# Performance work log

Hardware: AMD Instinct MI355X
Metric: run time of the kernel (lower is better)

Reference implementation:

```python
import jax, jax.numpy as jnp
import numpy as np

B, T, NQ, H = 32, 64, 128, 128


def setup_inputs() -> dict:
    key = jax.random.key(0)
    ks = jax.random.split(key, 16)
    n = lambda k, s, sc=0.05: jax.random.normal(k, s, dtype=jnp.float32) * sc
    return {
        "q": jax.random.randint(ks[0], (B, T), 0, NQ),
        "r": jax.random.randint(ks[1], (B, T), 0, 2),
        "x_emb_table": n(ks[2], (2 * NQ, H)),
        "q_emb": n(ks[3], (NQ, H)),
        "init_h": n(ks[4], (NQ, H)),
        "w1": n(ks[5], (H, 2 * H)),
        "b1": n(ks[6], (H,)),
        "w2": n(ks[7], (H, H)),
        "b2": n(ks[8], (H,)),
        "w_ih": n(ks[9], (3 * H, 2 * H)),
        "w_hh": n(ks[10], (3 * H, H)),
        "b_ih": n(ks[11], (3 * H,)),
        "b_hh": n(ks[12], (3 * H,)),
        "bias": n(ks[13], (1, NQ, 1)),
        "out_w": n(ks[14], (1, H)),
    }


def _gru_over_nodes(u, w_ih, w_hh, b_ih, b_hh):
    # Faithful to torch nn.GRU(batch_first=True) applied to [B, NQ, 2H]:
    # it recurs over the num_q axis with h0 = 0.
    h_dim = w_hh.shape[1]
    gi = jnp.einsum('bni,gi->bng', u, w_ih) + b_ih  # [B, NQ, 3H], input part precomputed

    def step(h, gi_t):  # h: [B, H], gi_t: [B, 3H]
        gh = h @ w_hh.T + b_hh
        ir, iz, inn = jnp.split(gi_t, 3, axis=-1)
        hr, hz, hn = jnp.split(gh, 3, axis=-1)
        rg = jax.nn.sigmoid(ir + hr)
        zg = jax.nn.sigmoid(iz + hz)
        ng = jnp.tanh(inn + rg * hn)
        h_new = (1.0 - zg) * ng + zg * h
        return h_new, h_new

    h0 = jnp.zeros((u.shape[0], h_dim), u.dtype)
    _, hs = jax.lax.scan(step, h0, jnp.swapaxes(gi, 0, 1))  # over NQ
    return jnp.swapaxes(hs, 0, 1)  # [B, NQ, H]


def reference(q, r, x_emb_table, q_emb, init_h, w1, b1, w2, b2,
              w_ih, w_hh, b_ih, b_hh, bias, out_w):
    bsz = q.shape[0]
    nq, hdim = q_emb.shape
    x = q + nq * r                                  # [B, T]
    x_emb = x_emb_table[x]                          # [B, T, H]
    qoh = jax.nn.one_hot(q, nq, dtype=x_emb.dtype)  # [B, T, NQ]
    ht0 = jnp.broadcast_to(init_h[None], (bsz, nq, hdim))

    def step(ht, inputs):
        xt, mask = inputs                # xt: [B,H], mask: [B,NQ]
        m3 = mask[..., None]             # [B, NQ, 1]
        # aggregate: second half is xt where qt matches, else q_emb; first half is ht either way
        other = m3 * xt[:, None, :] + (1.0 - m3) * q_emb[None]
        ht_ = jnp.concatenate([ht, other], axis=-1)          # [B, NQ, 2H]
        # update: f_neighbor is unimplemented (None->0); m = onehot * f_self(ht_)
        hs_mlp = jax.nn.relu(ht_ @ w1.T + b1) @ w2.T + b2    # mlp (eval: dropout=id)
        m = m3 * hs_mlp
        u = jnp.concatenate([m, ht], axis=-1)                # [B, NQ, 2H]
        ht_new = _gru_over_nodes(u, w_ih, w_hh, b_ih, b_hh)  # [B, NQ, H]
        yt = jax.nn.sigmoid(jnp.squeeze(ht_new @ out_w.T + bias, -1))  # [B, NQ]
        return ht_new, (ht_new, yt)

    _, (hs, ys) = jax.lax.scan(
        step, ht0, (jnp.swapaxes(x_emb, 0, 1), jnp.swapaxes(qoh, 0, 1)))
    h = jnp.concatenate([ht0[:, None], jnp.swapaxes(hs, 0, 1)], axis=1)  # [B, T+1, NQ, H]
    y = jnp.swapaxes(ys, 0, 1)                                           # [B, T, NQ]
    return y, h
```

## Files before the change

kernel.cpp:

```cpp
#include <hip/hip_runtime.h>

#define BB 32
#define TT 64
#define NQl 128
#define HD 128
#define CPAD 524
#define HPAD 132

#define SLOT_BYTES 8192
#define WS_FLAGS 8192
#define WS_SLOTS_OFF 16384
#define WS_NEED (WS_SLOTS_OFF + (size_t)NQl * SLOT_BYTES)

typedef _Float16 f16x8 __attribute__((ext_vector_type(8)));
typedef float f32x16 __attribute__((ext_vector_type(16)));
typedef float f32x4 __attribute__((ext_vector_type(4)));
typedef unsigned int u32x4 __attribute__((ext_vector_type(4)));
typedef int i32x4 __attribute__((ext_vector_type(4)));

__device__ __forceinline__ float sigmoidf_(float x) {
  return __builtin_amdgcn_rcpf(1.f + __expf(-x));
}
__device__ __forceinline__ float tanhf_(float x) {
  float a = fminf(fabsf(x), 15.f);
  float e = __expf(-2.f * a);
  float t = (1.f - e) * __builtin_amdgcn_rcpf(1.f + e);
  return copysignf(t, x);
}
__device__ __forceinline__ float dot4_(f32x4 a, f32x4 b) {
  return a[0] * b[0] + a[1] * b[1] + a[2] * b[2] + a[3] * b[3];
}
__device__ __forceinline__ f16x8 pack_frag_h(f32x4 a, f32x4 b) {
  f16x8 o;
  o[0] = (_Float16)a[0]; o[1] = (_Float16)a[1];
  o[2] = (_Float16)a[2]; o[3] = (_Float16)a[3];
  o[4] = (_Float16)b[0]; o[5] = (_Float16)b[1];
  o[6] = (_Float16)b[2]; o[7] = (_Float16)b[3];
  return o;
}
__device__ __forceinline__ u32x4 pack8_h(const float v[8]) {
  union { f16x8 h; u32x4 u; } c;
#pragma unroll
  for (int i = 0; i < 8; ++i) c.h[i] = (_Float16)v[i];
  return c.u;
}

__device__ __forceinline__ void bar_lds() {
  asm volatile("s_waitcnt lgkmcnt(0)" ::: "memory");
  __builtin_amdgcn_s_barrier();
  __builtin_amdgcn_sched_barrier(0);
}

__device__ __forceinline__ void issue_load32_cc(const float* p, f32x4& a, f32x4& b) {
  asm volatile(
      "global_load_dwordx4 %0, %2, off sc1\n\t"
      "global_load_dwordx4 %1, %2, off offset:16 sc1"
      : "=&v"(a), "=&v"(b) : "v"(p) : "memory");
}
__device__ __forceinline__ void wait_vm0_2(f32x4& a, f32x4& b) {
  asm volatile("s_waitcnt vmcnt(0)" : "+v"(a), "+v"(b) :: "memory");
  __builtin_amdgcn_sched_barrier(0);
}
__device__ __forceinline__ void store32_cc(float* p, f32x4 a, f32x4 b) {
  asm volatile(
      "global_store_dwordx4 %0, %1, off sc1\n\t"
      "global_store_dwordx4 %0, %2, off offset:16 sc1"
      :: "v"(p), "v"(a), "v"(b) : "memory");
}
__device__ __forceinline__ void issue_load16_cc(const void* p, u32x4& a) {
  asm volatile("global_load_dwordx4 %0, %1, off sc1" : "=&v"(a) : "v"(p) : "memory");
}
__device__ __forceinline__ void wait_vm0_1(u32x4& a) {
  asm volatile("s_waitcnt vmcnt(0)" : "+v"(a) :: "memory");
  __builtin_amdgcn_sched_barrier(0);
}
__device__ __forceinline__ void store16_cc(void* p, u32x4 v) {
  asm volatile("global_store_dwordx4 %0, %1, off sc1" :: "v"(p), "v"(v) : "memory");
}
__device__ __forceinline__ void store_flag_cc(int* p, int v) {
  asm volatile("global_store_dword %0, %1, off sc1" :: "v"(p), "v"(v) : "memory");
}
__device__ __forceinline__ int flagline_min(const int* p) {
  i32x4 a, b;
  asm volatile(
      "global_load_dwordx4 %0, %2, off sc1\n\t"
      "global_load_dwordx4 %1, %2, off offset:16 sc1\n\t"
      "s_waitcnt vmcnt(0)"
      : "=&v"(a), "=&v"(b) : "v"(p) : "memory");
  int m0 = min(min(a[0], a[1]), min(a[2], a[3]));
  int m1 = min(min(b[0], b[1]), min(b[2], b[3]));
  return min(m0, m1);
}

__global__ void __launch_bounds__(512, 2) gkt_wavefront(
    const int* __restrict__ qp, const int* __restrict__ rp_,
    const float* __restrict__ x_emb, const float* __restrict__ init_h,
    const float* __restrict__ w1, const float* __restrict__ b1,
    const float* __restrict__ w2, const float* __restrict__ b2,
    const float* __restrict__ w_ih, const float* __restrict__ w_hh,
    const float* __restrict__ b_ih, const float* __restrict__ b_hh,
    const float* __restrict__ bias, const float* __restrict__ out_w,
    float* __restrict__ y_out, float* h_out, int* wsbase,
    unsigned char* slots, int fastws) {
  __shared__ __align__(16) unsigned char smA[32 * 512];
  __shared__ float sC[32 * CPAD];
  __shared__ float sHrun[32 * HPAD];
  __shared__ float sHtp[2][32 * HPAD];
  __shared__ float sXt[32 * 128];
  __shared__ float sRed[4 * HPAD];
  __shared__ float sV1[128], sV2[128];
  __shared__ float sBias[128], sOutW[128], sB1[128], sB2[128];
  __shared__ unsigned int sMask[128];
  __shared__ int sTicket;

  const int tid = threadIdx.x;
  const int lane = tid & 63;
  const int wv = tid >> 6;
  const int l31 = lane & 31;
  const int lhi = lane >> 5;

  int* ticket = wsbase + 2048;
  if (tid == 0) sTicket = atomicAdd(ticket, 1);
  __syncthreads();
  const int t = sTicket;

  int* myFlagWord = (int*)((char*)wsbase + (size_t)t * 128) + wv;
  const int* parentLine = (const int*)((char*)wsbase + (size_t)(t - 1) * 128);

  if (tid < 128) {
    sBias[tid] = bias[tid];
    sOutW[tid] = out_w[tid];
    sB1[tid] = b1[tid];
    sB2[tid] = b2[tid];
    sMask[tid] = 0u;
  }
  for (int i = tid; i < 32 * HPAD; i += 512) sHrun[i] = 0.f;
  __syncthreads();
  if (tid < 32) {
    int qb = qp[tid * TT + t];
    atomicOr(&sMask[qb], 1u << tid);
  }

  const int b = tid >> 4;
  const int f = tid & 15;
  const unsigned int swzb = (unsigned int)((b & 7) << 4);
  const unsigned int imgOff = (unsigned int)(b * 256) + (((unsigned int)(f * 16)) ^ swzb);
  {
    int qb = qp[b * TT + t];
    int rb = rp_[b * TT + t];
    const float* src = x_emb + (size_t)(qb + NQl * rb) * HD + f * 8;
    *(f32x4*)(sXt + b * 128 + f * 8) = *(const f32x4*)src;
    *(f32x4*)(sXt + b * 128 + f * 8 + 4) = *(const f32x4*)(src + 4);
    *(u32x4*)(smA + b * 512 + ((unsigned int)(256 + f * 16) ^ swzb)) = (u32x4)(0u);
  }

  const int gcol = wv * 32 + l31;
  f16x8 Brz[16];
#pragma unroll
  for (int ks = 0; ks < 16; ++ks) {
    const float* src = (ks < 8)
        ? (w_ih + (size_t)gcol * 256 + 128 + ks * 16 + lhi * 8)
        : (w_hh + (size_t)gcol * 128 + (ks - 8) * 16 + lhi * 8);
    Brz[ks] = pack_frag_h(*(const f32x4*)src, *(const f32x4*)(src + 4));
  }
  const int ecol = (wv < 4) ? (256 + wv * 32 + l31) : (384 + (wv - 4) * 32 + l31);
  const int erow = (wv < 4) ? ecol : (ecol - 128);
  f16x8 Bex[8];
#pragma unroll
  for (int ks = 0; ks < 8; ++ks) {
    const float* src = (wv < 4)
        ? (w_ih + (size_t)erow * 256 + 128 + ks * 16 + lhi * 8)
        : (w_hh + (size_t)erow * 128 + ks * 16 + lhi * 8);
    Bex[ks] = pack_frag_h(*(const f32x4*)src, *(const f32x4*)(src + 4));
  }
  const float brz = b_ih[gcol] + b_hh[gcol];
  const float bex = (wv < 4) ? b_ih[ecol] : b_hh[erow];

  float* hstore_base = h_out + (((size_t)b * (TT + 1) + (t + 1)) * NQl) * HD + f * 8;
  const float* hload_base = h_out + (((size_t)b * (TT + 1) + t) * NQl) * HD + f * 8;

  {
    const f32x4* s4 = (const f32x4*)init_h;
    for (int i = t * 512 + tid; i < 32 * 4096; i += TT * 512) {
      int bb = i >> 12, rem = i & 4095;
      ((f32x4*)(h_out + ((size_t)bb * (TT + 1)) * NQl * HD))[rem] = s4[rem];
    }
  }

  {
    if (t > 0) {
      if (lane == 0) {
        int c = 0;
        while (flagline_min(parentLine) < 1) {
          if (++c > (1 << 17)) break;
        }
      }
      if (fastws) {
        u32x4 pv;
        issue_load16_cc(slots + imgOff, pv);
        wait_vm0_1(pv);
        *(u32x4*)(smA + b * 512 + (((unsigned int)(f * 16)) ^ swzb)) = pv;
        union { u32x4 u; _Float16 h[8]; } cc; cc.u = pv;
#pragma unroll
        for (int i = 0; i < 8; ++i) sHtp[0][b * HPAD + f * 8 + i] = (float)cc.h[i];
      } else {
        f32x4 a0, a1;
        issue_load32_cc(hload_base, a0, a1);
        wait_vm0_2(a0, a1);
        float v[8];
        *(f32x4*)&v[0] = a0; *(f32x4*)&v[4] = a1;
        *(f32x4*)(sHtp[0] + b * HPAD + f * 8) = a0;
        *(f32x4*)(sHtp[0] + b * HPAD + f * 8 + 4) = a1;
        *(u32x4*)(smA + b * 512 + (((unsigned int)(f * 16)) ^ swzb)) = pack8_h(v);
      }
    } else {
      float v[8];
      const float* src = init_h + f * 8;
      *(f32x4*)&v[0] = *(const f32x4*)src;
      *(f32x4*)&v[4] = *(const f32x4*)(src + 4);
      *(f32x4*)(sHtp[0] + b * HPAD + f * 8) = *(f32x4*)&v[0];
      *(f32x4*)(sHtp[0] + b * HPAD + f * 8 + 4) = *(f32x4*)&v[4];
      *(u32x4*)(smA + b * 512 + (((unsigned int)(f * 16)) ^ swzb)) = pack8_h(v);
    }
  }

  const int rowbase = l31 * 512;
  const unsigned int swz = (unsigned int)((l31 & 7) << 4);

  for (int n = 0; n < NQl; ++n) {
    bar_lds();

    f16x8 av[16];
#pragma unroll
    for (int ks = 0; ks < 16; ++ks) {
      unsigned int off = ((unsigned int)(ks * 32 + (lhi << 4))) ^ swz;
      av[ks] = *(const f16x8*)(smA + rowbase + off);
    }
    f32x16 accR, accE;
#pragma unroll
    for (int i = 0; i < 16; ++i) { accR[i] = brz; accE[i] = bex; }
#pragma unroll
    for (int ks = 0; ks < 16; ++ks)
      accR = __builtin_amdgcn_mfma_f32_32x32x16_f16(av[ks], Brz[ks], accR, 0, 0, 0);
    if (wv < 4) {
#pragma unroll
      for (int ks = 0; ks < 8; ++ks)
        accE = __builtin_amdgcn_mfma_f32_32x32x16_f16(av[ks], Bex[ks], accE, 0, 0, 0);
    } else {
#pragma unroll
      for (int ks = 0; ks < 8; ++ks)
        accE = __builtin_amdgcn_mfma_f32_32x32x16_f16(av[8 + ks], Bex[ks], accE, 0, 0, 0);
    }
#pragma unroll
    for (int rg = 0; rg < 16; ++rg) {
      int br = (rg & 3) + 8 * (rg >> 2) + 4 * lhi;
      sC[br * CPAD + gcol] = accR[rg];
      sC[br * CPAD + ecol] = accE[rg];
    }
    bar_lds();

    unsigned int mk = sMask[n];
    while (mk) {
      const int b0 = __ffs(mk) - 1;
      mk &= mk - 1;
      const float* htp_row = sHtp[n & 1] + b0 * HPAD;
      {
        const int j = tid & 127, kq = tid >> 7;
        const float* wr = w1 + (size_t)j * 256 + kq * 64;
        const float* xr = (kq < 2) ? (htp_row + kq * 64)
                                   : (sXt + b0 * 128 + (kq - 2) * 64);
        float s = 0.f;
#pragma unroll
        for (int ii = 0; ii < 16; ++ii)
          s += dot4_(*(const f32x4*)(wr + ii * 4), *(const f32x4*)(xr + ii * 4));
        sRed[kq * HPAD + j] = s;
      }
      bar_lds();
      if (tid < 128) {
        float v = sB1[tid] + sRed[tid] + sRed[HPAD + tid] + sRed[2 * HPAD + tid] +
                  sRed[3 * HPAD + tid];
        sV1[tid] = fmaxf(v, 0.f);
      }
      bar_lds();
      {
        const int j = tid & 127, kq = tid >> 7;
        const float* wr = w2 + (size_t)j * 128 + kq * 32;
        const float* xr = sV1 + kq * 32;
        float s = 0.f;
#pragma unroll
        for (int ii = 0; ii < 8; ++ii)
          s += dot4_(*(const f32x4*)(wr + ii * 4), *(const f32x4*)(xr + ii * 4));
        sRed[kq * HPAD + j] = s;
      }
      bar_lds();
      if (tid < 128)
        sV2[tid] = sB2[tid] + sRed[tid] + sRed[HPAD + tid] + sRed[2 * HPAD + tid] +
                   sRed[3 * HPAD + tid];
      bar_lds();
      if (tid < 384) {
        const float* wr = w_ih + (size_t)tid * 256;
        float s = 0.f;
#pragma unroll
        for (int ii = 0; ii < 32; ++ii)
          s += dot4_(*(const f32x4*)(wr + ii * 4), *(const f32x4*)(sV2 + ii * 4));
        sC[b0 * CPAD + tid] += s;
      }
      bar_lds();
    }

    float yp = 0.f;
    float hnew[8];
    {
      const int j0 = f * 8;
      const float* Cb = sC + b * CPAD;
      float rpre[8], zpre[8], ipre[8], hpre[8], hold[8];
      *(f32x4*)&rpre[0] = *(const f32x4*)(Cb + j0);
      *(f32x4*)&rpre[4] = *(const f32x4*)(Cb + j0 + 4);
      *(f32x4*)&zpre[0] = *(const f32x4*)(Cb + 128 + j0);
      *(f32x4*)&zpre[4] = *(const f32x4*)(Cb + 128 + j0 + 4);
      *(f32x4*)&ipre[0] = *(const f32x4*)(Cb + 256 + j0);
      *(f32x4*)&ipre[4] = *(const f32x4*)(Cb + 256 + j0 + 4);
      *(f32x4*)&hpre[0] = *(const f32x4*)(Cb + 384 + j0);
      *(f32x4*)&hpre[4] = *(const f32x4*)(Cb + 384 + j0 + 4);
      *(f32x4*)&hold[0] = *(const f32x4*)(sHrun + b * HPAD + j0);
      *(f32x4*)&hold[4] = *(const f32x4*)(sHrun + b * HPAD + j0 + 4);
#pragma unroll
      for (int i = 0; i < 8; ++i) {
        float rg = sigmoidf_(rpre[i]);
        float zg = sigmoidf_(zpre[i]);
        float ng = tanhf_(ipre[i] + rg * hpre[i]);
        float hv = ng + zg * (hold[i] - ng);
        hnew[i] = hv;
        yp += hv * sOutW[j0 + i];
      }
      *(f32x4*)(sHrun + b * HPAD + j0) = *(f32x4*)&hnew[0];
      *(f32x4*)(sHrun + b * HPAD + j0 + 4) = *(f32x4*)&hnew[4];
      u32x4 ph = pack8_h(hnew);
      *(u32x4*)(smA + b * 512 + ((unsigned int)(256 + f * 16) ^ swzb)) = ph;
      if (fastws) {
        store16_cc(slots + (size_t)n * SLOT_BYTES + imgOff, ph);
      } else {
        store32_cc(hstore_base + (size_t)n * HD, *(f32x4*)&hnew[0], *(f32x4*)&hnew[4]);
      }
    }

    asm volatile("s_waitcnt vmcnt(0)" ::: "memory");
    if (lane == 0) store_flag_cc(myFlagWord, n + 1);

    if (fastws) {
      float* hd = hstore_base + (size_t)n * HD;
      *(f32x4*)hd = *(const f32x4*)&hnew[0];
      *(f32x4*)(hd + 4) = *(const f32x4*)&hnew[4];
    }
    yp += __shfl_xor(yp, 1);
    yp += __shfl_xor(yp, 2);
    yp += __shfl_xor(yp, 4);
    yp += __shfl_xor(yp, 8);
    if (f == 0) {
      float yv = sigmoidf_(yp + sBias[n]);
      y_out[((size_t)b * TT + t) * NQl + n] = yv;
    }

    const int nn = n + 1;
    if (nn < NQl) {
      if (t > 0) {
        if (lane == 0) {
          int c = 0;
          while (flagline_min(parentLine) < nn + 1) {
            if (++c > (1 << 17)) break;
          }
        }
        if (fastws) {
          u32x4 pv;
          issue_load16_cc(slots + (size_t)nn * SLOT_BYTES + imgOff, pv);
          wait_vm0_1(pv);
          *(u32x4*)(smA + b * 512 + (((unsigned int)(f * 16)) ^ swzb)) = pv;
          union { u32x4 u; _Float16 h[8]; } cc; cc.u = pv;
#pragma unroll
          for (int i = 0; i < 8; ++i) sHtp[nn & 1][b * HPAD + f * 8 + i] = (float)cc.h[i];
        } else {
          f32x4 p0, p1;
          issue_load32_cc(hload_base + (size_t)nn * HD, p0, p1);
          wait_vm0_2(p0, p1);
          float v[8];
          *(f32x4*)&v[0] = p0; *(f32x4*)&v[4] = p1;
          *(f32x4*)(sHtp[nn & 1] + b * HPAD + f * 8) = p0;
          *(f32x4*)(sHtp[nn & 1] + b * HPAD + f * 8 + 4) = p1;
          *(u32x4*)(smA + b * 512 + (((unsigned int)(f * 16)) ^ swzb)) = pack8_h(v);
        }
      } else {
        float v[8];
        const float* src = init_h + (size_t)nn * HD + f * 8;
        *(f32x4*)&v[0] = *(const f32x4*)src;
        *(f32x4*)&v[4] = *(const f32x4*)(src + 4);
        *(f32x4*)(sHtp[nn & 1] + b * HPAD + f * 8) = *(f32x4*)&v[0];
        *(f32x4*)(sHtp[nn & 1] + b * HPAD + f * 8 + 4) = *(f32x4*)&v[4];
        *(u32x4*)(smA + b * 512 + (((unsigned int)(f * 16)) ^ swzb)) = pack8_h(v);
      }
    }
  }
}

extern "C" void kernel_launch(void* const* d_in, const int* in_sizes, int n_in,
                              void* d_out, int out_size, void* d_ws, size_t ws_size,
                              hipStream_t stream) {
  (void)in_sizes; (void)n_in; (void)out_size;
  const int* q = (const int*)d_in[0];
  const int* r = (const int*)d_in[1];
  const float* x_emb = (const float*)d_in[2];
  const float* init_h = (const float*)d_in[4];
  const float* w1 = (const float*)d_in[5];
  const float* b1 = (const float*)d_in[6];
  const float* w2 = (const float*)d_in[7];
  const float* b2 = (const float*)d_in[8];
  const float* w_ih = (const float*)d_in[9];
  const float* w_hh = (const float*)d_in[10];
  const float* b_ih = (const float*)d_in[11];
  const float* b_hh = (const float*)d_in[12];
  const float* bias = (const float*)d_in[13];
  const float* out_w = (const float*)d_in[14];

  float* y_out = (float*)d_out;
  float* h_out = y_out + (size_t)BB * TT * NQl;

  int* wsbase = (int*)d_ws;
  unsigned char* slots = (unsigned char*)d_ws + WS_SLOTS_OFF;
  const int fastws = (ws_size >= WS_NEED) ? 1 : 0;

  (void)hipMemsetAsync(d_ws, 0, WS_SLOTS_OFF, stream);
  gkt_wavefront<<<TT, 512, 0, stream>>>(q, r, x_emb, init_h, w1, b1, w2, b2,
                                        w_ih, w_hh, b_ih, b_hh, bias, out_w,
                                        y_out, h_out, wsbase, slots, fastws);
}
```

Baseline: 2.274 ms.

## Prefetch parent-step hidden rows two nodes ahead with double-buffered LDS A operand

Splits the LDS A-operand image into a double-buffered left half (parent ht rows) and a single right half (running GRU state). In the fast-workspace path, each block now waits on the parent's progress flag and issues relaxed loads for node n+2 while node n is processed, so the row for the next node is already in registers. This is meant to take the global-memory round trip and flag polling off the per-node critical path of the wavefront chain. In exchange it needs more registers and a cached progress counter, and it relies on the relaxed atomic loads being ordered after the flag check.

```diff
diff --git a/kernel.cpp b/kernel.cpp
--- a/kernel.cpp
+++ b/kernel.cpp
@@ -5,7 +5,6 @@
 #define NQl 128
 #define HD 128
 #define CPAD 524
-#define HPAD 132
 
 #define SLOT_BYTES 8192
 #define WS_FLAGS 8192
@@ -102,12 +101,13 @@
     const float* __restrict__ bias, const float* __restrict__ out_w,
     float* __restrict__ y_out, float* h_out, int* wsbase,
     unsigned char* slots, int fastws) {
-  __shared__ __align__(16) unsigned char smA[32 * 512];
+  __shared__ __align__(16) unsigned char smL[2][32 * 256];
+  __shared__ __align__(16) unsigned char smR[32 * 256];
   __shared__ float sC[32 * CPAD];
-  __shared__ float sHrun[32 * HPAD];
-  __shared__ float sHtp[2][32 * HPAD];
+  __shared__ float sHrun[32 * 128];
+  __shared__ float sHtp[2][32 * 128];
   __shared__ float sXt[32 * 128];
-  __shared__ float sRed[4 * HPAD];
+  __shared__ float sRed[4 * 132];
   __shared__ float sV1[128], sV2[128];
   __shared__ float sBias[128], sOutW[128], sB1[128], sB2[128];
   __shared__ unsigned int sMask[128];
@@ -134,7 +134,7 @@
     sB2[tid] = b2[tid];
     sMask[tid] = 0u;
   }
-  for (int i = tid; i < 32 * HPAD; i += 512) sHrun[i] = 0.f;
+  for (int i = tid; i < 32 * 128; i += 512) sHrun[i] = 0.f;
   __syncthreads();
   if (tid < 32) {
     int qb = qp[tid * TT + t];
@@ -144,14 +144,14 @@
   const int b = tid >> 4;
   const int f = tid & 15;
   const unsigned int swzb = (unsigned int)((b & 7) << 4);
-  const unsigned int imgOff = (unsigned int)(b * 256) + (((unsigned int)(f * 16)) ^ swzb);
+  const unsigned int rowOff = (unsigned int)(b * 256) + (((unsigned int)(f * 16)) ^ swzb);
   {
     int qb = qp[b * TT + t];
     int rb = rp_[b * TT + t];
     const float* src = x_emb + (size_t)(qb + NQl * rb) * HD + f * 8;
     *(f32x4*)(sXt + b * 128 + f * 8) = *(const f32x4*)src;
     *(f32x4*)(sXt + b * 128 + f * 8 + 4) = *(const f32x4*)(src + 4);
-    *(u32x4*)(smA + b * 512 + ((unsigned int)(256 + f * 16) ^ swzb)) = (u32x4)(0u);
+    *(u32x4*)(smR + rowOff) = (u32x4)(0u);
   }
 
   const int gcol = wv * 32 + l31;
@@ -187,54 +187,73 @@
     }
   }
 
+  int pprog = 0;
+  unsigned int sp0 = 0, sp1 = 0, sp2 = 0, sp3 = 0;
+
   {
     if (t > 0) {
       if (lane == 0) {
         int c = 0;
-        while (flagline_min(parentLine) < 1) {
+        while (pprog < 1) {
+          pprog = flagline_min(parentLine);
           if (++c > (1 << 17)) break;
         }
       }
       if (fastws) {
         u32x4 pv;
-        issue_load16_cc(slots + imgOff, pv);
+        issue_load16_cc(slots + rowOff, pv);
         wait_vm0_1(pv);
-        *(u32x4*)(smA + b * 512 + (((unsigned int)(f * 16)) ^ swzb)) = pv;
+        *(u32x4*)(smL[0] + rowOff) = pv;
         union { u32x4 u; _Float16 h[8]; } cc; cc.u = pv;
 #pragma unroll
-        for (int i = 0; i < 8; ++i) sHtp[0][b * HPAD + f * 8 + i] = (float)cc.h[i];
+        for (int i = 0; i < 8; ++i) sHtp[0][b * 128 + f * 8 + i] = (float)cc.h[i];
+        if (lane == 0) {
+          int c = 0;
+          while (pprog < 2) {
+            pprog = flagline_min(parentLine);
+            if (++c > (1 << 17)) break;
+          }
+        }
+        const unsigned int* sp = (const unsigned int*)(slots + SLOT_BYTES + rowOff);
+        sp0 = __hip_atomic_load(sp + 0, __ATOMIC_RELAXED, __HIP_MEMORY_SCOPE_AGENT);
+        sp1 = __hip_atomic_load(sp + 1, __ATOMIC_RELAXED, __HIP_MEMORY_SCOPE_AGENT);
+        sp2 = __hip_atomic_load(sp + 2, __ATOMIC_RELAXED, __HIP_MEMORY_SCOPE_AGENT);
+        sp3 = __hip_atomic_load(sp + 3, __ATOMIC_RELAXED, __HIP_MEMORY_SCOPE_AGENT);
       } else {
         f32x4 a0, a1;
         issue_load32_cc(hload_base, a0, a1);
         wait_vm0_2(a0, a1);
         float v[8];
         *(f32x4*)&v[0] = a0; *(f32x4*)&v[4] = a1;
-        *(f32x4*)(sHtp[0] + b * HPAD + f * 8) = a0;
-        *(f32x4*)(sHtp[0] + b * HPAD + f * 8 + 4) = a1;
-        *(u32x4*)(smA + b * 512 + (((unsigned int)(f * 16)) ^ swzb)) = pack8_h(v);
+        *(f32x4*)(sHtp[0] + b * 128 + f * 8) = a0;
+        *(f32x4*)(sHtp[0] + b * 128 + f * 8 + 4) = a1;
+        *(u32x4*)(smL[0] + rowOff) = pack8_h(v);
       }
     } else {
       float v[8];
       const float* src = init_h + f * 8;
       *(f32x4*)&v[0] = *(const f32x4*)src;
       *(f32x4*)&v[4] = *(const f32x4*)(src + 4);
-      *(f32x4*)(sHtp[0] + b * HPAD + f * 8) = *(f32x4*)&v[0];
-      *(f32x4*)(sHtp[0] + b * HPAD + f * 8 + 4) = *(f32x4*)&v[4];
-      *(u32x4*)(smA + b * 512 + (((unsigned int)(f * 16)) ^ swzb)) = pack8_h(v);
-    }
-  }
-
-  const int rowbase = l31 * 512;
+      *(f32x4*)(sHtp[0] + b * 128 + f * 8) = *(f32x4*)&v[0];
+      *(f32x4*)(sHtp[0] + b * 128 + f * 8 + 4) = *(f32x4*)&v[4];
+      *(u32x4*)(smL[0] + rowOff) = pack8_h(v);
+    }
+  }
+
+  const int rowbase = l31 * 256;
   const unsigned int swz = (unsigned int)((l31 & 7) << 4);
 
   for (int n = 0; n < NQl; ++n) {
+    const int nn = n + 1;
     bar_lds();
 
+    const unsigned char* smLcur = smL[n & 1];
     f16x8 av[16];
 #pragma unroll
-    for (int ks = 0; ks < 16; ++ks) {
+    for (int ks = 0; ks < 8; ++ks) {
       unsigned int off = ((unsigned int)(ks * 32 + (lhi << 4))) ^ swz;
-      av[ks] = *(const f16x8*)(smA + rowbase + off);
+      av[ks] = *(const f16x8*)(smLcur + rowbase + off);
+      av[8 + ks] = *(const f16x8*)(smR + rowbase + off);
     }
     f32x16 accR, accE;
 #pragma unroll
@@ -263,7 +282,7 @@
     while (mk) {
       const int b0 = __ffs(mk) - 1;
       mk &= mk - 1;
-      const float* htp_row = sHtp[n & 1] + b0 * HPAD;
+      const float* htp_row = sHtp[n & 1] + b0 * 128;
       {
         const int j = tid & 127, kq = tid >> 7;
         const float* wr = w1 + (size_t)j * 256 + kq * 64;
@@ -273,12 +292,12 @@
 #pragma unroll
         for (int ii = 0; ii < 16; ++ii)
           s += dot4_(*(const f32x4*)(wr + ii * 4), *(const f32x4*)(xr + ii * 4));
-        sRed[kq * HPAD + j] = s;
+        sRed[kq * 132 + j] = s;
       }
       bar_lds();
       if (tid < 128) {
-        float v = sB1[tid] + sRed[tid] + sRed[HPAD + tid] + sRed[2 * HPAD + tid] +
-                  sRed[3 * HPAD + tid];
+        float v = sB1[tid] + sRed[tid] + sRed[132 + tid] + sRed[2 * 132 + tid] +
+                  sRed[3 * 132 + tid];
         sV1[tid] = fmaxf(v, 0.f);
       }
       bar_lds();
@@ -290,12 +309,12 @@
 #pragma unroll
         for (int ii = 0; ii < 8; ++ii)
           s += dot4_(*(const f32x4*)(wr + ii * 4), *(const f32x4*)(xr + ii * 4));
-        sRed[kq * HPAD + j] = s;
+        sRed[kq * 132 + j] = s;
       }
       bar_lds();
       if (tid < 128)
-        sV2[tid] = sB2[tid] + sRed[tid] + sRed[HPAD + tid] + sRed[2 * HPAD + tid] +
-                   sRed[3 * HPAD + tid];
+        sV2[tid] = sB2[tid] + sRed[tid] + sRed[132 + tid] + sRed[2 * 132 + tid] +
+                   sRed[3 * 132 + tid];
       bar_lds();
       if (tid < 384) {
         const float* wr = w_ih + (size_t)tid * 256;
@@ -310,6 +329,7 @@
 
     float yp = 0.f;
     float hnew[8];
+    u32x4 ph;
     {
       const int j0 = f * 8;
       const float* Cb = sC + b * CPAD;
@@ -322,8 +342,8 @@
       *(f32x4*)&ipre[4] = *(const f32x4*)(Cb + 256 + j0 + 4);
       *(f32x4*)&hpre[0] = *(const f32x4*)(Cb + 384 + j0);
       *(f32x4*)&hpre[4] = *(const f32x4*)(Cb + 384 + j0 + 4);
-      *(f32x4*)&hold[0] = *(const f32x4*)(sHrun + b * HPAD + j0);
-      *(f32x4*)&hold[4] = *(const f32x4*)(sHrun + b * HPAD + j0 + 4);
+      *(f32x4*)&hold[0] = *(const f32x4*)(sHrun + b * 128 + j0);
+      *(f32x4*)&hold[4] = *(const f32x4*)(sHrun + b * 128 + j0 + 4);
 #pragma unroll
       for (int i = 0; i < 8; ++i) {
         float rg = sigmoidf_(rpre[i]);
@@ -333,12 +353,12 @@
         hnew[i] = hv;
         yp += hv * sOutW[j0 + i];
       }
-      *(f32x4*)(sHrun + b * HPAD + j0) = *(f32x4*)&hnew[0];
-      *(f32x4*)(sHrun + b * HPAD + j0 + 4) = *(f32x4*)&hnew[4];
-      u32x4 ph = pack8_h(hnew);
-      *(u32x4*)(smA + b * 512 + ((unsigned int)(256 + f * 16) ^ swzb)) = ph;
+      *(f32x4*)(sHrun + b * 128 + j0) = *(f32x4*)&hnew[0];
+      *(f32x4*)(sHrun + b * 128 + j0 + 4) = *(f32x4*)&hnew[4];
+      ph = pack8_h(hnew);
+      *(u32x4*)(smR + rowOff) = ph;
       if (fastws) {
-        store16_cc(slots + (size_t)n * SLOT_BYTES + imgOff, ph);
+        store16_cc(slots + (size_t)n * SLOT_BYTES + rowOff, ph);
       } else {
         store32_cc(hstore_base + (size_t)n * HD, *(f32x4*)&hnew[0], *(f32x4*)&hnew[4]);
       }
@@ -351,7 +371,67 @@
       float* hd = hstore_base + (size_t)n * HD;
       *(f32x4*)hd = *(const f32x4*)&hnew[0];
       *(f32x4*)(hd + 4) = *(const f32x4*)&hnew[4];
-    }
+      if (nn < NQl) {
+        u32x4 pv;
+        if (t > 0) {
+          pv[0] = sp0; pv[1] = sp1; pv[2] = sp2; pv[3] = sp3;
+        } else {
+          float v[8];
+          const float* src = init_h + (size_t)nn * HD + f * 8;
+          *(f32x4*)&v[0] = *(const f32x4*)src;
+          *(f32x4*)&v[4] = *(const f32x4*)(src + 4);
+          pv = pack8_h(v);
+        }
+        *(u32x4*)(smL[nn & 1] + rowOff) = pv;
+        union { u32x4 u; _Float16 h[8]; } cc; cc.u = pv;
+#pragma unroll
+        for (int i = 0; i < 8; ++i) sHtp[nn & 1][b * 128 + f * 8 + i] = (float)cc.h[i];
+      }
+      const int n2 = n + 2;
+      if (n2 < NQl && t > 0) {
+        if (lane == 0) {
+          int c = 0;
+          while (pprog < n2 + 1) {
+            pprog = flagline_min(parentLine);
+            if (++c > (1 << 17)) break;
+          }
+        }
+        const unsigned int* sp =
+            (const unsigned int*)(slots + (size_t)n2 * SLOT_BYTES + rowOff);
+        sp0 = __hip_atomic_load(sp + 0, __ATOMIC_RELAXED, __HIP_MEMORY_SCOPE_AGENT);
+        sp1 = __hip_atomic_load(sp + 1, __ATOMIC_RELAXED, __HIP_MEMORY_SCOPE_AGENT);
+        sp2 = __hip_atomic_load(sp + 2, __ATOMIC_RELAXED, __HIP_MEMORY_SCOPE_AGENT);
+        sp3 = __hip_atomic_load(sp + 3, __ATOMIC_RELAXED, __HIP_MEMORY_SCOPE_AGENT);
+      }
+    } else {
+      if (nn < NQl) {
+        if (t > 0) {
+          if (lane == 0) {
+            int c = 0;
+            while (flagline_min(parentLine) < nn + 1) {
+              if (++c > (1 << 17)) break;
+            }
+          }
+          f32x4 p0, p1;
+          issue_load32_cc(hload_base + (size_t)nn * HD, p0, p1);
+          wait_vm0_2(p0, p1);
+          float v[8];
+          *(f32x4*)&v[0] = p0; *(f32x4*)&v[4] = p1;
+          *(f32x4*)(sHtp[nn & 1] + b * 128 + f * 8) = p0;
+          *(f32x4*)(sHtp[nn & 1] + b * 128 + f * 8 + 4) = p1;
+          *(u32x4*)(smL[nn & 1] + rowOff) = pack8_h(v);
+        } else {
+          float v[8];
+          const float* src = init_h + (size_t)nn * HD + f * 8;
+          *(f32x4*)&v[0] = *(const f32x4*)src;
+          *(f32x4*)&v[4] = *(const f32x4*)(src + 4);
+          *(f32x4*)(sHtp[nn & 1] + b * 128 + f * 8) = *(f32x4*)&v[0];
+          *(f32x4*)(sHtp[nn & 1] + b * 128 + f * 8 + 4) = *(f32x4*)&v[4];
+          *(u32x4*)(smL[nn & 1] + rowOff) = pack8_h(v);
+        }
+      }
+    }
+
     yp += __shfl_xor(yp, 1);
     yp += __shfl_xor(yp, 2);
     yp += __shfl_xor(yp, 4);
@@ -359,44 +439,6 @@
     if (f == 0) {
       float yv = sigmoidf_(yp + sBias[n]);
       y_out[((size_t)b * TT + t) * NQl + n] = yv;
-    }
-
-    const int nn = n + 1;
-    if (nn < NQl) {
-      if (t > 0) {
-        if (lane == 0) {
-          int c = 0;
-          while (flagline_min(parentLine) < nn + 1) {
-            if (++c > (1 << 17)) break;
-          }
-        }
-        if (fastws) {
-          u32x4 pv;
-          issue_load16_cc(slots + (size_t)nn * SLOT_BYTES + imgOff, pv);
-          wait_vm0_1(pv);
-          *(u32x4*)(smA + b * 512 + (((unsigned int)(f * 16)) ^ swzb)) = pv;
-          union { u32x4 u; _Float16 h[8]; } cc; cc.u = pv;
-#pragma unroll
-          for (int i = 0; i < 8; ++i) sHtp[nn & 1][b * HPAD + f * 8 + i] = (float)cc.h[i];
-        } else {
-          f32x4 p0, p1;
-          issue_load32_cc(hload_base + (size_t)nn * HD, p0, p1);
-          wait_vm0_2(p0, p1);
-          float v[8];
-          *(f32x4*)&v[0] = p0; *(f32x4*)&v[4] = p1;
-          *(f32x4*)(sHtp[nn & 1] + b * HPAD + f * 8) = p0;
-          *(f32x4*)(sHtp[nn & 1] + b * HPAD + f * 8 + 4) = p1;
-          *(u32x4*)(smA + b * 512 + (((unsigned int)(f * 16)) ^ swzb)) = pack8_h(v);
-        }
-      } else {
-        float v[8];
-        const float* src = init_h + (size_t)nn * HD + f * 8;
-        *(f32x4*)&v[0] = *(const f32x4*)src;
-        *(f32x4*)&v[4] = *(const f32x4*)(src + 4);
-        *(f32x4*)(sHtp[nn & 1] + b * HPAD + f * 8) = *(f32x4*)&v[0];
-        *(f32x4*)(sHtp[nn & 1] + b * HPAD + f * 8 + 4) = *(f32x4*)&v[4];
-        *(u32x4*)(smA + b * 512 + (((unsigned int)(f * 16)) ^ swzb)) = pack8_h(v);
-      }
     }
   }
 }
```

New measurement: 2.869 ms. 1.26x slower.
